# Kernel tuning notes

Hardware: AMD Instinct MI355X
Metric: run time of the kernel (lower is better)

The kernel has to match this reference:

```python
import jax, jax.numpy as jnp
import numpy as np

B, T, C = 2, 2048, 1024
H = 16
HD = C // H  # 64


def setup_inputs() -> dict:
    key = jax.random.key(0)
    k1, k2, k3, k4, k5 = jax.random.split(key, 5)
    s = 0.02
    return {
        "x": jax.random.normal(k1, (B, T, C), dtype=jnp.float32),
        "w_attn": jax.random.normal(k2, (C, 3 * C), dtype=jnp.float32) * s,
        "b_attn": jnp.zeros((3 * C,), dtype=jnp.float32),
        "w_proj": jax.random.normal(k3, (C, C), dtype=jnp.float32) * s,
        "b_proj": jnp.zeros((C,), dtype=jnp.float32),
    }


def reference(x, w_attn, b_attn, w_proj, b_proj):
    Bx, Tx, Cx = x.shape
    qkv = x @ w_attn + b_attn                      # [B,T,3C]
    q, k, v = jnp.split(qkv, 3, axis=-1)
    # [B,T,C] -> [B,H,T,HD]
    def heads(t):
        return t.reshape(Bx, Tx, H, HD).transpose(0, 2, 1, 3)
    q, k, v = heads(q), heads(k), heads(v)
    scale = 1.0 / np.sqrt(HD).astype(np.float32)
    scores = jnp.einsum("bhqd,bhkd->bhqk", q, k) * scale
    causal = jnp.tril(jnp.ones((Tx, Tx), dtype=bool))
    scores = jnp.where(causal, scores, -jnp.inf)
    attn = jax.nn.softmax(scores, axis=-1)          # dropout p=0 -> identity
    y = jnp.einsum("bhqk,bhkd->bhqd", attn, v)
    y = y.transpose(0, 2, 1, 3).reshape(Bx, Tx, Cx)
    return y @ w_proj + b_proj
```

## Files before the change

kernel.cpp:

```cpp
#include <hip/hip_runtime.h>
#include <hip/hip_bf16.h>

#define Bb 2
#define Tt 2048
#define Cc 1024
#define Hh 16
#define HD 64
#define QS 0.18033688f

typedef __attribute__((ext_vector_type(8))) short bf16x8;
typedef __attribute__((ext_vector_type(4))) short bf16x4;
typedef __attribute__((ext_vector_type(4))) float f32x4;
typedef __attribute__((ext_vector_type(2))) unsigned int u32x2;

__device__ inline short f2b(float f) {
    unsigned int u = __builtin_bit_cast(unsigned int, f);
    unsigned int r = (u + 0x7FFFu + ((u >> 16) & 1u)) >> 16;
    return (short)(unsigned short)r;
}

__device__ inline void gl16(const void* g, void* l) {
    __builtin_amdgcn_global_load_lds(
        (const __attribute__((address_space(1))) void*)g,
        (__attribute__((address_space(3))) void*)l, 16, 0, 0);
}

__global__ __launch_bounds__(256) void cvt_kernel(const float* __restrict__ in,
                                                  short* __restrict__ outb) {
    int i = (blockIdx.x * 256 + threadIdx.x) * 8;
    float4 a = *(const float4*)(in + i);
    float4 b = *(const float4*)(in + i + 4);
    bf16x8 v;
    v[0] = f2b(a.x); v[1] = f2b(a.y); v[2] = f2b(a.z); v[3] = f2b(a.w);
    v[4] = f2b(b.x); v[5] = f2b(b.y); v[6] = f2b(b.z); v[7] = f2b(b.w);
    *(bf16x8*)(outb + i) = v;
}

__global__ __launch_bounds__(256) void twt_kernel(const float* __restrict__ W,
                                                  short* __restrict__ WT,
                                                  int K, int N) {
    int k0 = blockIdx.x * 64, n0 = blockIdx.y * 64;
    int nl = threadIdx.x & 63, kg = threadIdx.x >> 6;
    int n = n0 + nl;
    short v[16];
#pragma unroll
    for (int i = 0; i < 16; i++) {
        int k = k0 + kg * 16 + i;
        v[i] = f2b(W[(size_t)k * N + n]);
    }
    short* dst = WT + (size_t)n * K + k0 + kg * 16;
    *(bf16x8*)dst = *(bf16x8*)&v[0];
    *(bf16x8*)(dst + 8) = *(bf16x8*)&v[8];
}

__global__ __launch_bounds__(256) void gemm_qkv(
    const short* __restrict__ A, const short* __restrict__ Bt,
    const float* __restrict__ bias,
    short* __restrict__ qw, short* __restrict__ kw, short* __restrict__ vTw,
    int M, int N, int K)
{
    __shared__ __attribute__((aligned(16))) short As[128 * 32];
    __shared__ __attribute__((aligned(16))) short Bs[128 * 32];

    const int tid  = threadIdx.x;
    const int wave = tid >> 6, lane = tid & 63;
    const int quad = lane >> 4, lr = lane & 15;
    const int wm = wave >> 1, wn = wave & 1;
    const int m0 = blockIdx.y * 128, n0 = blockIdx.x * 128;
    const int rowo = lane >> 2, kco = (lane & 3) << 3;

    f32x4 acc[4][4];
    const f32x4 zf = {0.f, 0.f, 0.f, 0.f};
#pragma unroll
    for (int mi = 0; mi < 4; mi++)
#pragma unroll
        for (int ni = 0; ni < 4; ni++) acc[mi][ni] = zf;

    for (int k0 = 0; k0 < K; k0 += 32) {
        __syncthreads();
#pragma unroll
        for (int i = 0; i < 2; i++) {
            int c = wave + i * 4;
            int row = c * 16 + rowo;
            gl16(A + (size_t)(m0 + row) * K + k0 + kco, &As[c * 512 + lane * 8]);
            gl16(Bt + (size_t)(n0 + row) * K + k0 + kco, &Bs[c * 512 + lane * 8]);
        }
        __syncthreads();

        bf16x8 af[4], bf[4];
#pragma unroll
        for (int mi = 0; mi < 4; mi++)
            af[mi] = *(bf16x8*)&As[(wm * 64 + mi * 16 + lr) * 32 + quad * 8];
#pragma unroll
        for (int ni = 0; ni < 4; ni++)
            bf[ni] = *(bf16x8*)&Bs[(wn * 64 + ni * 16 + lr) * 32 + quad * 8];
#pragma unroll
        for (int mi = 0; mi < 4; mi++)
#pragma unroll
            for (int ni = 0; ni < 4; ni++)
                acc[mi][ni] = __builtin_amdgcn_mfma_f32_16x16x32_bf16(
                    af[mi], bf[ni], acc[mi][ni], 0, 0, 0);
    }

#pragma unroll
    for (int mi = 0; mi < 4; mi++) {
#pragma unroll
        for (int ni = 0; ni < 4; ni++) {
            int c = n0 + wn * 64 + ni * 16 + lr;
            float bv = bias[c];
#pragma unroll
            for (int r = 0; r < 4; r++) {
                int rg = m0 + wm * 64 + mi * 16 + quad * 4 + r;
                float val = acc[mi][ni][r] + bv;
                int which = c >> 10, cc = c & 1023;
                int h = cc >> 6, d = cc & 63;
                int b = rg >> 11, t = rg & 2047;
                size_t bh = (size_t)b * Hh + h;
                if (which == 0)      qw[(bh * Tt + t) * HD + d] = f2b(val * QS);
                else if (which == 1) kw[(bh * Tt + t) * HD + d] = f2b(val);
                else                 vTw[(bh * HD + d) * Tt + t] = f2b(val);
            }
        }
    }
}

__global__ __launch_bounds__(256) void gemm_proj(
    const short* __restrict__ A, const short* __restrict__ Bt,
    const float* __restrict__ bias, float* __restrict__ out,
    int M, int N, int K)
{
    __shared__ __attribute__((aligned(16))) short As[64 * 32];
    __shared__ __attribute__((aligned(16))) short Bs[128 * 32];

    const int tid  = threadIdx.x;
    const int wave = tid >> 6, lane = tid & 63;
    const int quad = lane >> 4, lr = lane & 15;
    const int wm = wave >> 1, wn = wave & 1;
    const int m0 = blockIdx.y * 64, n0 = blockIdx.x * 128;

    f32x4 acc[2][4];
    const f32x4 zf = {0.f, 0.f, 0.f, 0.f};
#pragma unroll
    for (int mi = 0; mi < 2; mi++)
#pragma unroll
        for (int ni = 0; ni < 4; ni++) acc[mi][ni] = zf;

    for (int k0 = 0; k0 < K; k0 += 32) {
        __syncthreads();
        {
            int row = tid >> 2, kc = (tid & 3) << 3;
            int rg = m0 + row, b = rg >> 11, t = rg & 2047;
            int c = k0 + kc, h = c >> 6, d = c & 63;
            gl16(A + ((((size_t)b * Hh + h) * Tt + t) * HD + d), &As[tid * 8]);
        }
#pragma unroll
        for (int i = 0; i < 2; i++) {
            int id = i * 256 + tid;
            int row = id >> 2, kc = (id & 3) << 3;
            gl16(Bt + (size_t)(n0 + row) * K + k0 + kc, &Bs[id * 8]);
        }
        __syncthreads();

        bf16x8 af[2], bf[4];
#pragma unroll
        for (int mi = 0; mi < 2; mi++)
            af[mi] = *(bf16x8*)&As[(wm * 32 + mi * 16 + lr) * 32 + quad * 8];
#pragma unroll
        for (int ni = 0; ni < 4; ni++)
            bf[ni] = *(bf16x8*)&Bs[(wn * 64 + ni * 16 + lr) * 32 + quad * 8];
#pragma unroll
        for (int mi = 0; mi < 2; mi++)
#pragma unroll
            for (int ni = 0; ni < 4; ni++)
                acc[mi][ni] = __builtin_amdgcn_mfma_f32_16x16x32_bf16(
                    af[mi], bf[ni], acc[mi][ni], 0, 0, 0);
    }

#pragma unroll
    for (int mi = 0; mi < 2; mi++)
#pragma unroll
        for (int ni = 0; ni < 4; ni++) {
            int c = n0 + wn * 64 + ni * 16 + lr;
            float bv = bias[c];
#pragma unroll
            for (int r = 0; r < 4; r++) {
                int rg = m0 + wm * 32 + mi * 16 + quad * 4 + r;
                out[(size_t)rg * N + c] = acc[mi][ni][r] + bv;
            }
        }
}

__global__ __launch_bounds__(256) void gemm_f32src(
    const void* __restrict__ Araw, const float* __restrict__ Bm,
    const float* __restrict__ bias, float* __restrict__ out,
    short* __restrict__ qw, short* __restrict__ kw, short* __restrict__ vTw,
    int M, int N, int K, int mode)
{
    __shared__ __attribute__((aligned(16))) short As[128 * 32];
    __shared__ __attribute__((aligned(16))) short Bs[128 * 32];

    const int tid  = threadIdx.x;
    const int wave = tid >> 6, lane = tid & 63;
    const int quad = lane >> 4, lr = lane & 15;
    const int wm = wave >> 1, wn = wave & 1;
    const int m0 = blockIdx.y * 128, n0 = blockIdx.x * 128;

    f32x4 acc[4][4];
    const f32x4 zf = {0.f, 0.f, 0.f, 0.f};
#pragma unroll
    for (int mi = 0; mi < 4; mi++)
#pragma unroll
        for (int ni = 0; ni < 4; ni++) acc[mi][ni] = zf;

    for (int k0 = 0; k0 < K; k0 += 32) {
        __syncthreads();
        if (mode == 1) {
            const float* Af = (const float*)Araw;
#pragma unroll
            for (int i = 0; i < 4; i++) {
                int id  = i * 256 + tid;
                int row = id >> 3;
                int kc  = (id & 7) << 2;
                float4 v = *(const float4*)(Af + (size_t)(m0 + row) * K + k0 + kc);
                short* d = &As[row * 32 + kc];
                d[0] = f2b(v.x); d[1] = f2b(v.y); d[2] = f2b(v.z); d[3] = f2b(v.w);
            }
        } else {
            const short* Ah = (const short*)Araw;
#pragma unroll
            for (int i = 0; i < 2; i++) {
                int id  = i * 256 + tid;
                int row = id >> 2;
                int kc  = (id & 3) << 3;
                int rg = m0 + row, b = rg >> 11, t = rg & 2047;
                int c = k0 + kc, h = c >> 6, d = c & 63;
                *(bf16x8*)&As[row * 32 + kc] =
                    *(const bf16x8*)(Ah + ((((size_t)b * Hh + h) * Tt + t) * HD + d));
            }
        }
#pragma unroll
        for (int i = 0; i < 4; i++) {
            int id = i * 256 + tid;
            int kr = id >> 5;
            int nc = (id & 31) << 2;
            float4 v = *(const float4*)(Bm + (size_t)(k0 + kr) * N + n0 + nc);
            Bs[(nc + 0) * 32 + kr] = f2b(v.x);
            Bs[(nc + 1) * 32 + kr] = f2b(v.y);
            Bs[(nc + 2) * 32 + kr] = f2b(v.z);
            Bs[(nc + 3) * 32 + kr] = f2b(v.w);
        }
        __syncthreads();

        bf16x8 af[4], bf[4];
#pragma unroll
        for (int mi = 0; mi < 4; mi++)
            af[mi] = *(bf16x8*)&As[(wm * 64 + mi * 16 + lr) * 32 + quad * 8];
#pragma unroll
        for (int ni = 0; ni < 4; ni++)
            bf[ni] = *(bf16x8*)&Bs[(wn * 64 + ni * 16 + lr) * 32 + quad * 8];
#pragma unroll
        for (int mi = 0; mi < 4; mi++)
#pragma unroll
            for (int ni = 0; ni < 4; ni++)
                acc[mi][ni] = __builtin_amdgcn_mfma_f32_16x16x32_bf16(
                    af[mi], bf[ni], acc[mi][ni], 0, 0, 0);
    }

#pragma unroll
    for (int mi = 0; mi < 4; mi++) {
#pragma unroll
        for (int ni = 0; ni < 4; ni++) {
            int c = n0 + wn * 64 + ni * 16 + lr;
            float bv = bias[c];
#pragma unroll
            for (int r = 0; r < 4; r++) {
                int rg = m0 + wm * 64 + mi * 16 + quad * 4 + r;
                float val = acc[mi][ni][r] + bv;
                if (mode == 1) {
                    int which = c >> 10, cc = c & 1023;
                    int h = cc >> 6, d = cc & 63;
                    int b = rg >> 11, t = rg & 2047;
                    size_t bh = (size_t)b * Hh + h;
                    if (which == 0)      qw[(bh * Tt + t) * HD + d] = f2b(val * QS);
                    else if (which == 1) kw[(bh * Tt + t) * HD + d] = f2b(val);
                    else                 vTw[(bh * HD + d) * Tt + t] = f2b(val);
                } else {
                    out[(size_t)rg * N + c] = val;
                }
            }
        }
    }
}

__global__ __launch_bounds__(256) void attn_kernel(
    short* __restrict__ qw, const short* __restrict__ kw,
    const short* __restrict__ vTw)
{
    __shared__ __attribute__((aligned(16))) short Ks[2][64 * 64];
    __shared__ __attribute__((aligned(16))) short Vs[2][64 * 64];

    const int bh = blockIdx.x & 31;
    const int tile = 15 - (blockIdx.x >> 5);
    const int q0 = tile * 128;
    const int tid = threadIdx.x;
    const int wave = tid >> 6, lane = tid & 63;
    const int quad = lane >> 4, lr = lane & 15;
    const int r0w = q0 + wave * 32;

    short* qp = qw + (size_t)bh * Tt * HD;
    const short* kp = kw + (size_t)bh * Tt * HD;
    const short* vp = vTw + (size_t)bh * HD * Tt;

    int srow[2], scol[2];
#pragma unroll
    for (int i = 0; i < 2; i++) {
        int id = i * 256 + tid;
        srow[i] = id >> 3;
        scol[i] = ((id & 7) ^ (srow[i] & 7)) << 3;
    }

    bf16x8 aq[2][2];
#pragma unroll
    for (int mt = 0; mt < 2; mt++)
#pragma unroll
        for (int h = 0; h < 2; h++)
            aq[mt][h] = *(const bf16x8*)(qp + (size_t)(r0w + mt * 16 + lr) * HD
                                            + h * 32 + quad * 8);

    const f32x4 zf = {0.f, 0.f, 0.f, 0.f};
    f32x4 o[2][4];
    float lacc[2] = {0.f, 0.f};
#pragma unroll
    for (int mt = 0; mt < 2; mt++)
#pragma unroll
        for (int nt = 0; nt < 4; nt++) o[mt][nt] = zf;

#pragma unroll
    for (int i = 0; i < 2; i++) {
        gl16(kp + (size_t)srow[i] * HD + scol[i], &Ks[0][(i * 256 + tid) * 8]);
        gl16(vp + (size_t)srow[i] * Tt + scol[i], &Vs[0][(i * 256 + tid) * 8]);
    }

    const int jlast = q0 + 64;
    int it = 0;
    for (int j0 = 0; j0 <= jlast; j0 += 64, ++it) {
        const int cur = it & 1;
        __syncthreads();
        if (j0 < jlast) {
#pragma unroll
            for (int i = 0; i < 2; i++) {
                gl16(kp + (size_t)(j0 + 64 + srow[i]) * HD + scol[i],
                     &Ks[cur ^ 1][(i * 256 + tid) * 8]);
                gl16(vp + (size_t)srow[i] * Tt + (j0 + 64) + scol[i],
                     &Vs[cur ^ 1][(i * 256 + tid) * 8]);
            }
        }
        if (j0 <= r0w + 31) {
            const short* Kc = &Ks[cur][0];
            const short* Vc = &Vs[cur][0];
            const bool needmask = (j0 + 63 > r0w);
#pragma unroll
            for (int kt = 0; kt < 4; kt++) {
                if (j0 + kt * 16 > r0w + 31) break;
                int krow = (kt * 16 + lr) * 8;
                bf16x8 kb0 = *(const bf16x8*)&Kc[(krow + (quad ^ (lr & 7))) * 8];
                bf16x8 kb1 = *(const bf16x8*)&Kc[(krow + ((4 + quad) ^ (lr & 7))) * 8];
                bf16x4 va[4];
#pragma unroll
                for (int nt = 0; nt < 4; nt++) {
                    int vrow = (nt * 16 + lr) * 8;
                    int slot = (kt * 2 + (quad >> 1)) ^ (lr & 7);
                    va[nt] = *(const bf16x4*)&Vc[(vrow + slot) * 8 + (quad & 1) * 4];
                }
#pragma unroll
                for (int mt = 0; mt < 2; mt++) {
                    f32x4 s = __builtin_amdgcn_mfma_f32_16x16x32_bf16(
                        kb0, aq[mt][0], zf, 0, 0, 0);
                    s = __builtin_amdgcn_mfma_f32_16x16x32_bf16(
                        kb1, aq[mt][1], s, 0, 0, 0);
                    unsigned u[4];
#pragma unroll
                    for (int r = 0; r < 4; r++) {
                        float e = __builtin_amdgcn_exp2f(s[r]);
                        if (needmask &&
                            (j0 + kt * 16 + quad * 4 + r) > (r0w + mt * 16 + lr))
                            e = 0.f;
                        u[r] = __builtin_bit_cast(unsigned, e);
                        lacc[mt] += __builtin_bit_cast(float, u[r] & 0xFFFF0000u);
                    }
                    u32x2 pu = { __builtin_amdgcn_perm(u[1], u[0], 0x07060302u),
                                 __builtin_amdgcn_perm(u[3], u[2], 0x07060302u) };
                    bf16x4 pt = __builtin_bit_cast(bf16x4, pu);
#pragma unroll
                    for (int nt = 0; nt < 4; nt++)
                        o[mt][nt] = __builtin_amdgcn_mfma_f32_16x16x16bf16_1k(
                            va[nt], pt, o[mt][nt], 0, 0, 0);
                }
            }
        }
    }

#pragma unroll
    for (int mt = 0; mt < 2; mt++) {
        lacc[mt] += __shfl_xor(lacc[mt], 16, 64);
        lacc[mt] += __shfl_xor(lacc[mt], 32, 64);
        lacc[mt] = 1.0f / lacc[mt];
    }

#pragma unroll
    for (int mt = 0; mt < 2; mt++)
#pragma unroll
        for (int nt = 0; nt < 4; nt++) {
            bf16x4 ov;
#pragma unroll
            for (int r = 0; r < 4; r++) ov[r] = f2b(o[mt][nt][r] * lacc[mt]);
            *(bf16x4*)(qp + (size_t)(r0w + mt * 16 + lr) * HD + nt * 16 + quad * 4) = ov;
        }
}

extern "C" void kernel_launch(void* const* d_in, const int* in_sizes, int n_in,
                              void* d_out, int out_size, void* d_ws, size_t ws_size,
                              hipStream_t stream) {
    const float* x      = (const float*)d_in[0];
    const float* w_attn = (const float*)d_in[1];
    const float* b_attn = (const float*)d_in[2];
    const float* w_proj = (const float*)d_in[3];
    const float* b_proj = (const float*)d_in[4];
    float* out = (float*)d_out;

    const size_t per = (size_t)Bb * Hh * Tt * HD;
    short* qw  = (short*)d_ws;
    short* kw  = qw + per;
    short* vTw = kw + per;
    const int M = Bb * Tt;

    const size_t need_fast = (3 * per + per + (size_t)3072 * 1024 + (size_t)1024 * 1024) * 2;

    if (ws_size >= need_fast) {
        short* xbf = vTw + per;
        short* wAT = xbf + per;
        short* wPT = wAT + (size_t)3072 * 1024;

        cvt_kernel<<<dim3((int)(per / (256 * 8))), 256, 0, stream>>>(x, xbf);
        twt_kernel<<<dim3(Cc / 64, 3 * Cc / 64), 256, 0, stream>>>(w_attn, wAT, Cc, 3 * Cc);
        twt_kernel<<<dim3(Cc / 64, Cc / 64), 256, 0, stream>>>(w_proj, wPT, Cc, Cc);

        gemm_qkv<<<dim3(3 * Cc / 128, M / 128), 256, 0, stream>>>(
            xbf, wAT, b_attn, qw, kw, vTw, M, 3 * Cc, Cc);

        attn_kernel<<<dim3(512), 256, 0, stream>>>(qw, kw, vTw);

        gemm_proj<<<dim3(Cc / 128, M / 64), 256, 0, stream>>>(
            qw, wPT, b_proj, out, M, Cc, Cc);
    } else {
        gemm_f32src<<<dim3(3 * Cc / 128, M / 128), 256, 0, stream>>>(
            x, w_attn, b_attn, nullptr, qw, kw, vTw, M, 3 * Cc, Cc, 1);

        attn_kernel<<<dim3(512), 256, 0, stream>>>(qw, kw, vTw);

        gemm_f32src<<<dim3(Cc / 128, M / 128), 256, 0, stream>>>(
            qw, w_proj, b_proj, out, nullptr, nullptr, nullptr, M, Cc, Cc, 2);
    }
}
```

Measured before the change: 206.1 us.

## Merge prep kernels, deepen QKV GEMM K-tile with swizzle, balance causal attention blocks

Three conversion/transposition launches are merged into one prep kernel to cut launch overhead. The QKV GEMM now loads a 64-wide K slab per iteration with an XOR-swizzled LDS layout, halving barriers and reducing bank conflicts. The attention kernel switches to 128-thread blocks that each process a pair of query strips (p and 63-p), so causal work is balanced across blocks. This doubles the block count. It also adds per-strip activity checks inside the key loop.

```diff
diff --git a/kernel.cpp b/kernel.cpp
--- a/kernel.cpp
+++ b/kernel.cpp
@@ -25,29 +25,33 @@
         (__attribute__((address_space(3))) void*)l, 16, 0, 0);
 }
 
-__global__ __launch_bounds__(256) void cvt_kernel(const float* __restrict__ in,
-                                                  short* __restrict__ outb) {
-    int i = (blockIdx.x * 256 + threadIdx.x) * 8;
-    float4 a = *(const float4*)(in + i);
-    float4 b = *(const float4*)(in + i + 4);
-    bf16x8 v;
-    v[0] = f2b(a.x); v[1] = f2b(a.y); v[2] = f2b(a.z); v[3] = f2b(a.w);
-    v[4] = f2b(b.x); v[5] = f2b(b.y); v[6] = f2b(b.z); v[7] = f2b(b.w);
-    *(bf16x8*)(outb + i) = v;
-}
-
-__global__ __launch_bounds__(256) void twt_kernel(const float* __restrict__ W,
-                                                  short* __restrict__ WT,
-                                                  int K, int N) {
-    int k0 = blockIdx.x * 64, n0 = blockIdx.y * 64;
-    int nl = threadIdx.x & 63, kg = threadIdx.x >> 6;
+__global__ __launch_bounds__(256) void prep_kernel(
+    const float* __restrict__ x, short* __restrict__ xbf,
+    const float* __restrict__ wA, short* __restrict__ wAT,
+    const float* __restrict__ wP, short* __restrict__ wPT)
+{
+    const int bx = blockIdx.x, tid = threadIdx.x;
+    if (bx < 2048) {
+        int i = (bx * 256 + tid) * 8;
+        float4 a = *(const float4*)(x + i);
+        float4 b = *(const float4*)(x + i + 4);
+        bf16x8 v;
+        v[0] = f2b(a.x); v[1] = f2b(a.y); v[2] = f2b(a.z); v[3] = f2b(a.w);
+        v[4] = f2b(b.x); v[5] = f2b(b.y); v[6] = f2b(b.z); v[7] = f2b(b.w);
+        *(bf16x8*)(xbf + i) = v;
+        return;
+    }
+    const float* W; short* WT; int N, t;
+    if (bx < 2816) { t = bx - 2048; W = wA; WT = wAT; N = 3072; }
+    else           { t = bx - 2816; W = wP; WT = wPT; N = 1024; }
+    const int K = 1024;
+    int k0 = (t & 15) * 64, n0 = (t >> 4) * 64;
+    int nl = tid & 63, kg = tid >> 6;
     int n = n0 + nl;
     short v[16];
 #pragma unroll
-    for (int i = 0; i < 16; i++) {
-        int k = k0 + kg * 16 + i;
-        v[i] = f2b(W[(size_t)k * N + n]);
-    }
+    for (int i = 0; i < 16; i++)
+        v[i] = f2b(W[(size_t)(k0 + kg * 16 + i) * N + n]);
     short* dst = WT + (size_t)n * K + k0 + kg * 16;
     *(bf16x8*)dst = *(bf16x8*)&v[0];
     *(bf16x8*)(dst + 8) = *(bf16x8*)&v[8];
@@ -59,15 +63,22 @@
     short* __restrict__ qw, short* __restrict__ kw, short* __restrict__ vTw,
     int M, int N, int K)
 {
-    __shared__ __attribute__((aligned(16))) short As[128 * 32];
-    __shared__ __attribute__((aligned(16))) short Bs[128 * 32];
+    __shared__ __attribute__((aligned(16))) short As[128 * 64];
+    __shared__ __attribute__((aligned(16))) short Bs[128 * 64];
 
     const int tid  = threadIdx.x;
     const int wave = tid >> 6, lane = tid & 63;
     const int quad = lane >> 4, lr = lane & 15;
     const int wm = wave >> 1, wn = wave & 1;
     const int m0 = blockIdx.y * 128, n0 = blockIdx.x * 128;
-    const int rowo = lane >> 2, kco = (lane & 3) << 3;
+
+    int srow[4], scol[4];
+#pragma unroll
+    for (int i = 0; i < 4; i++) {
+        int id = i * 256 + tid;
+        srow[i] = id >> 3;
+        scol[i] = ((id & 7) ^ (srow[i] & 7)) << 3;
+    }
 
     f32x4 acc[4][4];
     const f32x4 zf = {0.f, 0.f, 0.f, 0.f};
@@ -76,30 +87,37 @@
 #pragma unroll
         for (int ni = 0; ni < 4; ni++) acc[mi][ni] = zf;
 
-    for (int k0 = 0; k0 < K; k0 += 32) {
-        __syncthreads();
-#pragma unroll
-        for (int i = 0; i < 2; i++) {
-            int c = wave + i * 4;
-            int row = c * 16 + rowo;
-            gl16(A + (size_t)(m0 + row) * K + k0 + kco, &As[c * 512 + lane * 8]);
-            gl16(Bt + (size_t)(n0 + row) * K + k0 + kco, &Bs[c * 512 + lane * 8]);
-        }
-        __syncthreads();
-
-        bf16x8 af[4], bf[4];
-#pragma unroll
-        for (int mi = 0; mi < 4; mi++)
-            af[mi] = *(bf16x8*)&As[(wm * 64 + mi * 16 + lr) * 32 + quad * 8];
-#pragma unroll
-        for (int ni = 0; ni < 4; ni++)
-            bf[ni] = *(bf16x8*)&Bs[(wn * 64 + ni * 16 + lr) * 32 + quad * 8];
-#pragma unroll
-        for (int mi = 0; mi < 4; mi++)
-#pragma unroll
-            for (int ni = 0; ni < 4; ni++)
-                acc[mi][ni] = __builtin_amdgcn_mfma_f32_16x16x32_bf16(
-                    af[mi], bf[ni], acc[mi][ni], 0, 0, 0);
+    for (int k0 = 0; k0 < K; k0 += 64) {
+        __syncthreads();
+#pragma unroll
+        for (int i = 0; i < 4; i++) {
+            gl16(A + (size_t)(m0 + srow[i]) * K + k0 + scol[i],
+                 &As[(i * 256 + tid) * 8]);
+            gl16(Bt + (size_t)(n0 + srow[i]) * K + k0 + scol[i],
+                 &Bs[(i * 256 + tid) * 8]);
+        }
+        __syncthreads();
+
+#pragma unroll
+        for (int ks = 0; ks < 2; ks++) {
+            bf16x8 af[4], bf[4];
+#pragma unroll
+            for (int mi = 0; mi < 4; mi++) {
+                int row = wm * 64 + mi * 16 + lr;
+                af[mi] = *(bf16x8*)&As[(row * 8 + ((ks * 4 + quad) ^ (lr & 7))) * 8];
+            }
+#pragma unroll
+            for (int ni = 0; ni < 4; ni++) {
+                int row = wn * 64 + ni * 16 + lr;
+                bf[ni] = *(bf16x8*)&Bs[(row * 8 + ((ks * 4 + quad) ^ (lr & 7))) * 8];
+            }
+#pragma unroll
+            for (int mi = 0; mi < 4; mi++)
+#pragma unroll
+                for (int ni = 0; ni < 4; ni++)
+                    acc[mi][ni] = __builtin_amdgcn_mfma_f32_16x16x32_bf16(
+                        af[mi], bf[ni], acc[mi][ni], 0, 0, 0);
+        }
     }
 
 #pragma unroll
@@ -292,29 +310,30 @@
     }
 }
 
-__global__ __launch_bounds__(256) void attn_kernel(
+__global__ __launch_bounds__(128) void attn_kernel(
     short* __restrict__ qw, const short* __restrict__ kw,
     const short* __restrict__ vTw)
 {
-    __shared__ __attribute__((aligned(16))) short Ks[2][64 * 64];
-    __shared__ __attribute__((aligned(16))) short Vs[2][64 * 64];
+    __shared__ __attribute__((aligned(16))) short Ks[2][4096];
+    __shared__ __attribute__((aligned(16))) short Vs[2][4096];
 
     const int bh = blockIdx.x & 31;
-    const int tile = 15 - (blockIdx.x >> 5);
-    const int q0 = tile * 128;
+    const int p  = blockIdx.x >> 5;
+    const int pB = 63 - p;
     const int tid = threadIdx.x;
     const int wave = tid >> 6, lane = tid & 63;
     const int quad = lane >> 4, lr = lane & 15;
-    const int r0w = q0 + wave * 32;
 
     short* qp = qw + (size_t)bh * Tt * HD;
     const short* kp = kw + (size_t)bh * Tt * HD;
     const short* vp = vTw + (size_t)bh * HD * Tt;
 
-    int srow[2], scol[2];
-#pragma unroll
-    for (int i = 0; i < 2; i++) {
-        int id = i * 256 + tid;
+    const int r0m[2] = { p * 32 + wave * 16, pB * 32 + wave * 16 };
+
+    int srow[4], scol[4];
+#pragma unroll
+    for (int i = 0; i < 4; i++) {
+        int id = i * 128 + tid;
         srow[i] = id >> 3;
         scol[i] = ((id & 7) ^ (srow[i] & 7)) << 3;
     }
@@ -324,7 +343,7 @@
     for (int mt = 0; mt < 2; mt++)
 #pragma unroll
         for (int h = 0; h < 2; h++)
-            aq[mt][h] = *(const bf16x8*)(qp + (size_t)(r0w + mt * 16 + lr) * HD
+            aq[mt][h] = *(const bf16x8*)(qp + (size_t)(r0m[mt] + lr) * HD
                                             + h * 32 + quad * 8);
 
     const f32x4 zf = {0.f, 0.f, 0.f, 0.f};
@@ -336,66 +355,66 @@
         for (int nt = 0; nt < 4; nt++) o[mt][nt] = zf;
 
 #pragma unroll
-    for (int i = 0; i < 2; i++) {
-        gl16(kp + (size_t)srow[i] * HD + scol[i], &Ks[0][(i * 256 + tid) * 8]);
-        gl16(vp + (size_t)srow[i] * Tt + scol[i], &Vs[0][(i * 256 + tid) * 8]);
-    }
-
-    const int jlast = q0 + 64;
-    int it = 0;
-    for (int j0 = 0; j0 <= jlast; j0 += 64, ++it) {
-        const int cur = it & 1;
-        __syncthreads();
-        if (j0 < jlast) {
-#pragma unroll
-            for (int i = 0; i < 2; i++) {
+    for (int i = 0; i < 4; i++) {
+        gl16(kp + (size_t)srow[i] * HD + scol[i], &Ks[0][(i * 128 + tid) * 8]);
+        gl16(vp + (size_t)srow[i] * Tt + scol[i], &Vs[0][(i * 128 + tid) * 8]);
+    }
+
+    const int clast = (pB * 32 + 31) >> 6;
+    for (int c = 0; c <= clast; ++c) {
+        const int j0 = c << 6;
+        const int cur = c & 1;
+        __syncthreads();
+        if (c < clast) {
+#pragma unroll
+            for (int i = 0; i < 4; i++) {
                 gl16(kp + (size_t)(j0 + 64 + srow[i]) * HD + scol[i],
-                     &Ks[cur ^ 1][(i * 256 + tid) * 8]);
+                     &Ks[cur ^ 1][(i * 128 + tid) * 8]);
                 gl16(vp + (size_t)srow[i] * Tt + (j0 + 64) + scol[i],
-                     &Vs[cur ^ 1][(i * 256 + tid) * 8]);
-            }
-        }
-        if (j0 <= r0w + 31) {
-            const short* Kc = &Ks[cur][0];
-            const short* Vc = &Vs[cur][0];
-            const bool needmask = (j0 + 63 > r0w);
-#pragma unroll
-            for (int kt = 0; kt < 4; kt++) {
-                if (j0 + kt * 16 > r0w + 31) break;
-                int krow = (kt * 16 + lr) * 8;
-                bf16x8 kb0 = *(const bf16x8*)&Kc[(krow + (quad ^ (lr & 7))) * 8];
-                bf16x8 kb1 = *(const bf16x8*)&Kc[(krow + ((4 + quad) ^ (lr & 7))) * 8];
-                bf16x4 va[4];
-#pragma unroll
-                for (int nt = 0; nt < 4; nt++) {
-                    int vrow = (nt * 16 + lr) * 8;
-                    int slot = (kt * 2 + (quad >> 1)) ^ (lr & 7);
-                    va[nt] = *(const bf16x4*)&Vc[(vrow + slot) * 8 + (quad & 1) * 4];
+                     &Vs[cur ^ 1][(i * 128 + tid) * 8]);
+            }
+        }
+        const short* Kc = &Ks[cur][0];
+        const short* Vc = &Vs[cur][0];
+#pragma unroll
+        for (int kt = 0; kt < 4; kt++) {
+            const int k16 = j0 + kt * 16;
+            const bool act0 = k16 <= r0m[0] + 15;
+            const bool act1 = k16 <= r0m[1] + 15;
+            if (!act1 && !act0) break;
+            int krow = (kt * 16 + lr) * 8;
+            bf16x8 kb0 = *(const bf16x8*)&Kc[(krow + (quad ^ (lr & 7))) * 8];
+            bf16x8 kb1 = *(const bf16x8*)&Kc[(krow + ((4 + quad) ^ (lr & 7))) * 8];
+            bf16x4 va[4];
+#pragma unroll
+            for (int nt = 0; nt < 4; nt++) {
+                int vrow = (nt * 16 + lr) * 8;
+                int slot = (kt * 2 + (quad >> 1)) ^ (lr & 7);
+                va[nt] = *(const bf16x4*)&Vc[(vrow + slot) * 8 + (quad & 1) * 4];
+            }
+#pragma unroll
+            for (int mt = 0; mt < 2; mt++) {
+                if (!(mt ? act1 : act0)) continue;
+                f32x4 s = __builtin_amdgcn_mfma_f32_16x16x32_bf16(
+                    kb0, aq[mt][0], zf, 0, 0, 0);
+                s = __builtin_amdgcn_mfma_f32_16x16x32_bf16(
+                    kb1, aq[mt][1], s, 0, 0, 0);
+                const bool needmask = (k16 + 15) > r0m[mt];
+                unsigned u[4];
+#pragma unroll
+                for (int r = 0; r < 4; r++) {
+                    float e = __builtin_amdgcn_exp2f(s[r]);
+                    if (needmask && (k16 + quad * 4 + r) > (r0m[mt] + lr)) e = 0.f;
+                    u[r] = __builtin_bit_cast(unsigned, e);
+                    lacc[mt] += __builtin_bit_cast(float, u[r] & 0xFFFF0000u);
                 }
-#pragma unroll
-                for (int mt = 0; mt < 2; mt++) {
-                    f32x4 s = __builtin_amdgcn_mfma_f32_16x16x32_bf16(
-                        kb0, aq[mt][0], zf, 0, 0, 0);
-                    s = __builtin_amdgcn_mfma_f32_16x16x32_bf16(
-                        kb1, aq[mt][1], s, 0, 0, 0);
-                    unsigned u[4];
-#pragma unroll
-                    for (int r = 0; r < 4; r++) {
-                        float e = __builtin_amdgcn_exp2f(s[r]);
-                        if (needmask &&
-                            (j0 + kt * 16 + quad * 4 + r) > (r0w + mt * 16 + lr))
-                            e = 0.f;
-                        u[r] = __builtin_bit_cast(unsigned, e);
-                        lacc[mt] += __builtin_bit_cast(float, u[r] & 0xFFFF0000u);
-                    }
-                    u32x2 pu = { __builtin_amdgcn_perm(u[1], u[0], 0x07060302u),
-                                 __builtin_amdgcn_perm(u[3], u[2], 0x07060302u) };
-                    bf16x4 pt = __builtin_bit_cast(bf16x4, pu);
-#pragma unroll
-                    for (int nt = 0; nt < 4; nt++)
-                        o[mt][nt] = __builtin_amdgcn_mfma_f32_16x16x16bf16_1k(
-                            va[nt], pt, o[mt][nt], 0, 0, 0);
-                }
+                u32x2 pu = { __builtin_amdgcn_perm(u[1], u[0], 0x07060302u),
+                             __builtin_amdgcn_perm(u[3], u[2], 0x07060302u) };
+                bf16x4 pt = __builtin_bit_cast(bf16x4, pu);
+#pragma unroll
+                for (int nt = 0; nt < 4; nt++)
+                    o[mt][nt] = __builtin_amdgcn_mfma_f32_16x16x16bf16_1k(
+                        va[nt], pt, o[mt][nt], 0, 0, 0);
             }
         }
     }
@@ -414,7 +433,7 @@
             bf16x4 ov;
 #pragma unroll
             for (int r = 0; r < 4; r++) ov[r] = f2b(o[mt][nt][r] * lacc[mt]);
-            *(bf16x4*)(qp + (size_t)(r0w + mt * 16 + lr) * HD + nt * 16 + quad * 4) = ov;
+            *(bf16x4*)(qp + (size_t)(r0m[mt] + lr) * HD + nt * 16 + quad * 4) = ov;
         }
 }
 
@@ -441,14 +460,12 @@
         short* wAT = xbf + per;
         short* wPT = wAT + (size_t)3072 * 1024;
 
-        cvt_kernel<<<dim3((int)(per / (256 * 8))), 256, 0, stream>>>(x, xbf);
-        twt_kernel<<<dim3(Cc / 64, 3 * Cc / 64), 256, 0, stream>>>(w_attn, wAT, Cc, 3 * Cc);
-        twt_kernel<<<dim3(Cc / 64, Cc / 64), 256, 0, stream>>>(w_proj, wPT, Cc, Cc);
+        prep_kernel<<<dim3(3072), 256, 0, stream>>>(x, xbf, w_attn, wAT, w_proj, wPT);
 
         gemm_qkv<<<dim3(3 * Cc / 128, M / 128), 256, 0, stream>>>(
             xbf, wAT, b_attn, qw, kw, vTw, M, 3 * Cc, Cc);
 
-        attn_kernel<<<dim3(512), 256, 0, stream>>>(qw, kw, vTw);
+        attn_kernel<<<dim3(1024), 128, 0, stream>>>(qw, kw, vTw);
 
         gemm_proj<<<dim3(Cc / 128, M / 64), 256, 0, stream>>>(
             qw, wPT, b_proj, out, M, Cc, Cc);
@@ -456,7 +473,7 @@
         gemm_f32src<<<dim3(3 * Cc / 128, M / 128), 256, 0, stream>>>(
             x, w_attn, b_attn, nullptr, qw, kw, vTw, M, 3 * Cc, Cc, 1);
 
-        attn_kernel<<<dim3(512), 256, 0, stream>>>(qw, kw, vTw);
+        attn_kernel<<<dim3(1024), 128, 0, stream>>>(qw, kw, vTw);
 
         gemm_f32src<<<dim3(Cc / 128, M / 128), 256, 0, stream>>>(
             qw, w_proj, b_proj, out, nullptr, nullptr, nullptr, M, Cc, Cc, 2);
```

Measured after the change: 215.0 us. 4.3% more time.
